# Performance work log

Measured on AMD Instinct MI355X. Metric: run time of the kernel, lower is better.

Reference implementation:

```python
import jax, jax.numpy as jnp
import numpy as np

N_NODES = 100000


def _sage_conv(x, src, dst, wn, ws, b):
    # mean-aggregate neighbor messages at destination nodes
    msgs = x[src]                                        # [E, D] gather
    agg = jax.ops.segment_sum(msgs, dst, num_segments=N_NODES)
    deg = jax.ops.segment_sum(jnp.ones((src.shape[0],), x.dtype), dst,
                              num_segments=N_NODES)
    agg = agg / jnp.maximum(deg, 1.0)[:, None]
    return agg @ wn + x @ ws + b


def setup_inputs() -> dict:
    key = jax.random.key(0)
    k = jax.random.split(key, 5)
    D = 128
    E = 1600000
    EL = 200000
    return {
        "node_features": jax.random.normal(k[0], (N_NODES, D), jnp.float32),
        "edge_index": jax.random.randint(k[1], (2, E), 0, N_NODES, jnp.int64),
        "edge_label_index": jax.random.randint(k[2], (2, EL), 0, N_NODES, jnp.int64),
        "w_neigh": jax.random.normal(k[3], (3, D, D), jnp.float32) * (1.0 / np.sqrt(D)),
        "w_self": jax.random.normal(k[4], (3, D, D), jnp.float32) * (1.0 / np.sqrt(D)),
        "bias": jnp.zeros((3, D), jnp.float32),
    }


def reference(node_features, edge_index, edge_label_index, w_neigh, w_self, bias):
    src, dst = edge_index[0], edge_index[1]
    # layer 0: conv -> relu (dropout is identity in eval mode)
    h = _sage_conv(node_features, src, dst, w_neigh[0], w_self[0], bias[0])
    h = jax.nn.relu(h)
    # middle layer: conv + residual -> relu
    h = jax.nn.relu(_sage_conv(h, src, dst, w_neigh[1], w_self[1], bias[1]) + h)
    # last layer: conv + residual (hidden_dim == output_dim, no projection)
    h = _sage_conv(h, src, dst, w_neigh[2], w_self[2], bias[2]) + h
    # dot-product link decoder
    logits = jnp.sum(h[edge_label_index[0]] * h[edge_label_index[1]], axis=-1)
    return logits
```

## Files before the change

kernel.cpp:

```cpp
#include <hip/hip_runtime.h>
#include <cstdint>
#include <cstddef>

#define D 128

typedef _Float16 half8 __attribute__((ext_vector_type(8)));
typedef float f32x4 __attribute__((ext_vector_type(4)));

static __device__ __forceinline__ unsigned short f2h_bits(float f) {
    union { _Float16 h; unsigned short u; } c;
    c.h = (_Float16)f;
    return c.u;
}

__global__ void hist_kernel(const int* __restrict__ dst, int E,
                            int* __restrict__ counts) {
    int i = blockIdx.x * blockDim.x + threadIdx.x;
    if (i < E) atomicAdd(&counts[dst[i]], 1);
}

__global__ void block_sum_kernel(const int* __restrict__ counts, int n,
                                 int* __restrict__ bsum) {
    __shared__ int sh[256];
    int t = threadIdx.x;
    int i = blockIdx.x * 256 + t;
    sh[t] = (i < n) ? counts[i] : 0;
    __syncthreads();
    for (int off = 128; off; off >>= 1) {
        if (t < off) sh[t] += sh[t + off];
        __syncthreads();
    }
    if (t == 0) bsum[blockIdx.x] = sh[0];
}

__global__ void scan_small_kernel(int* __restrict__ bsum, int nb,
                                  int* __restrict__ row_ptr, int N, int E) {
    __shared__ int sh[512];
    int t = threadIdx.x;
    int v = (t < nb) ? bsum[t] : 0;
    sh[t] = v;
    __syncthreads();
    for (int off = 1; off < 512; off <<= 1) {
        int add = (t >= off) ? sh[t - off] : 0;
        __syncthreads();
        sh[t] += add;
        __syncthreads();
    }
    if (t < nb) bsum[t] = sh[t] - v;
    if (t == 0) row_ptr[N] = E;
}

__global__ void block_scan_kernel(const int* __restrict__ counts, int n,
                                  const int* __restrict__ bsum,
                                  int* __restrict__ row_ptr) {
    __shared__ int sh[256];
    int t = threadIdx.x;
    int i = blockIdx.x * 256 + t;
    int v = (i < n) ? counts[i] : 0;
    sh[t] = v;
    __syncthreads();
    for (int off = 1; off < 256; off <<= 1) {
        int add = (t >= off) ? sh[t - off] : 0;
        __syncthreads();
        sh[t] += add;
        __syncthreads();
    }
    if (i < n) row_ptr[i] = bsum[blockIdx.x] + sh[t] - v;
}

__global__ void fill_kernel(const int* __restrict__ src,
                            const int* __restrict__ dst, int E,
                            const int* __restrict__ row_ptr,
                            int* __restrict__ cursor,
                            int* __restrict__ csr_src) {
    int i = blockIdx.x * blockDim.x + threadIdx.x;
    if (i < E) {
        int d = dst[i];
        int pos = row_ptr[d] + atomicAdd(&cursor[d], 1);
        csr_src[pos] = src[i];
    }
}

__global__ void f32_to_f16(const float* __restrict__ in,
                           unsigned short* __restrict__ out, int n8) {
    int i = blockIdx.x * 256 + threadIdx.x;
    if (i >= n8) return;
    float4 f0 = ((const float4*)in)[2 * i];
    float4 f1 = ((const float4*)in)[2 * i + 1];
    union { unsigned short u[8]; uint4 v; } o;
    o.u[0] = f2h_bits(f0.x); o.u[1] = f2h_bits(f0.y);
    o.u[2] = f2h_bits(f0.z); o.u[3] = f2h_bits(f0.w);
    o.u[4] = f2h_bits(f1.x); o.u[5] = f2h_bits(f1.y);
    o.u[6] = f2h_bits(f1.z); o.u[7] = f2h_bits(f1.w);
    ((uint4*)out)[i] = o.v;
}

__global__ __launch_bounds__(256) void gather_agg16(
    const unsigned short* __restrict__ h16, const int* __restrict__ row_ptr,
    const int* __restrict__ csr_src,
    unsigned short* __restrict__ agg16, int N) {
    int node = (int)((blockIdx.x * (size_t)blockDim.x + threadIdx.x) >> 6);
    int lane = threadIdx.x & 63;
    if (node >= N) return;
    int beg = row_ptr[node], end = row_ptr[node + 1];
    const int col = lane * 2;
    float ax[8], ay[8];
#pragma unroll
    for (int j = 0; j < 8; j++) { ax[j] = 0.f; ay[j] = 0.f; }
    int e = beg;
    for (; e + 8 <= end; e += 8) {
        int s[8];
#pragma unroll
        for (int j = 0; j < 8; j++) s[j] = csr_src[e + j];
        unsigned int v[8];
#pragma unroll
        for (int j = 0; j < 8; j++)
            v[j] = *(const unsigned int*)(h16 + (size_t)s[j] * D + col);
#pragma unroll
        for (int j = 0; j < 8; j++) {
            union { unsigned int u; _Float16 h[2]; } c; c.u = v[j];
            ax[j] += (float)c.h[0];
            ay[j] += (float)c.h[1];
        }
    }
    for (; e < end; ++e) {
        int s = csr_src[e];
        union { unsigned int u; _Float16 h[2]; } c;
        c.u = *(const unsigned int*)(h16 + (size_t)s * D + col);
        ax[0] += (float)c.h[0];
        ay[0] += (float)c.h[1];
    }
    float sx = (ax[0] + ax[1]) + (ax[2] + ax[3]) + (ax[4] + ax[5]) + (ax[6] + ax[7]);
    float sy = (ay[0] + ay[1]) + (ay[2] + ay[3]) + (ay[4] + ay[5]) + (ay[6] + ay[7]);
    float sc = 1.0f / fmaxf((float)(end - beg), 1.0f);
    union { unsigned int u; _Float16 h[2]; } o;
    o.h[0] = (_Float16)(sx * sc);
    o.h[1] = (_Float16)(sy * sc);
    *(unsigned int*)(agg16 + (size_t)node * D + col) = o.u;
}

__global__ void wprep_kernel(const float* __restrict__ wn,
                             const float* __restrict__ wsf,
                             unsigned short* __restrict__ wh,
                             unsigned short* __restrict__ wl) {
    int idx = blockIdx.x * 256 + threadIdx.x;
    int L = idx >> 15;
    int rem = idx & 32767;
    int n = rem >> 8;
    int k = rem & 255;
    float w = (k < 128) ? wn[L * 16384 + k * 128 + n]
                        : wsf[L * 16384 + (k - 128) * 128 + n];
    _Float16 hi = (_Float16)w;
    _Float16 lo = (_Float16)(w - (float)hi);
    union { _Float16 h; unsigned short u; } ch, cl;
    ch.h = hi; cl.h = lo;
    wh[idx] = ch.u;
    wl[idx] = cl.u;
}

template <bool RELU, bool RES, bool F32OUT>
__global__ __launch_bounds__(256) void gemm_mfma16(
    const unsigned short* __restrict__ agg16,
    const unsigned short* __restrict__ h16self,
    const unsigned short* __restrict__ res16,
    const unsigned short* __restrict__ wh,
    const unsigned short* __restrict__ wl,
    const float* __restrict__ bias,
    float* __restrict__ hout,
    unsigned short* __restrict__ h16out,
    int N) {
    const int t = threadIdx.x;
    const int wv = t >> 6;
    const int lane = t & 63;
    const int r = lane & 15;
    const int q = lane >> 4;
    const int m0 = blockIdx.x * 128 + (wv >> 1) * 64;
    const int n0 = (wv & 1) * 64;

    int rowA[4];
#pragma unroll
    for (int mt = 0; mt < 4; mt++) {
        int rr = m0 + mt * 16 + r;
        rowA[mt] = (rr < N) ? rr : (N - 1);
    }

    f32x4 acc[4][4];
#pragma unroll
    for (int mt = 0; mt < 4; mt++)
#pragma unroll
        for (int nt = 0; nt < 4; nt++) acc[mt][nt] = (f32x4){0.f, 0.f, 0.f, 0.f};

#pragma unroll
    for (int kb = 0; kb < 8; kb++) {
        const unsigned short* base = (kb < 4) ? agg16 : h16self;
        const int ko = (kb & 3) * 32 + q * 8;
        half8 a[4];
#pragma unroll
        for (int mt = 0; mt < 4; mt++)
            a[mt] = *(const half8*)(base + (size_t)rowA[mt] * D + ko);
        const int wko = kb * 32 + q * 8;
#pragma unroll
        for (int nt = 0; nt < 4; nt++) {
            const size_t wo = (size_t)(n0 + nt * 16 + r) * 256 + wko;
            half8 whv = *(const half8*)(wh + wo);
            half8 wlv = *(const half8*)(wl + wo);
#pragma unroll
            for (int mt = 0; mt < 4; mt++) {
                acc[mt][nt] = __builtin_amdgcn_mfma_f32_16x16x32_f16(
                    a[mt], whv, acc[mt][nt], 0, 0, 0);
                acc[mt][nt] = __builtin_amdgcn_mfma_f32_16x16x32_f16(
                    a[mt], wlv, acc[mt][nt], 0, 0, 0);
            }
        }
    }

#pragma unroll
    for (int nt = 0; nt < 4; nt++) {
        const int col = n0 + nt * 16 + r;
        const float bv = bias[col];
#pragma unroll
        for (int mt = 0; mt < 4; mt++) {
#pragma unroll
            for (int reg = 0; reg < 4; reg++) {
                int row = m0 + mt * 16 + q * 4 + reg;
                if (row >= N) continue;
                float o = acc[mt][nt][reg] + bv;
                if (RES)
                    o += (float)(*(const _Float16*)(res16 + (size_t)row * D + col));
                if (RELU) o = fmaxf(o, 0.f);
                if (F32OUT) hout[(size_t)row * D + col] = o;
                else        h16out[(size_t)row * D + col] = f2h_bits(o);
            }
        }
    }
}

__global__ void decoder_kernel(const float* __restrict__ h,
                               const int* __restrict__ eli, int EL,
                               float* __restrict__ out) {
    long long tid = (long long)blockIdx.x * blockDim.x + threadIdx.x;
    int lane = (int)(tid & 31);
    long long e = tid >> 5;
    if (e >= EL) return;
    int u = eli[e];
    int v = eli[e + EL];
    float4 a = *(const float4*)(h + (long long)u * D + lane * 4);
    float4 b = *(const float4*)(h + (long long)v * D + lane * 4);
    float p = a.x * b.x + a.y * b.y + a.z * b.z + a.w * b.w;
#pragma unroll
    for (int off = 16; off; off >>= 1) p += __shfl_xor(p, off);
    if (lane == 0) out[e] = p;
}

static inline size_t align256(size_t x) { return (x + 255) & ~(size_t)255; }

extern "C" void kernel_launch(void* const* d_in, const int* in_sizes, int n_in,
                              void* d_out, int out_size, void* d_ws,
                              size_t ws_size, hipStream_t stream) {
    const float* x    = (const float*)d_in[0];
    const int*   ei   = (const int*)d_in[1];
    const int*   eli  = (const int*)d_in[2];
    const float* wn   = (const float*)d_in[3];
    const float* wsf  = (const float*)d_in[4];
    const float* bias = (const float*)d_in[5];

    const int N  = in_sizes[0] / D;
    const int E  = in_sizes[1] / 2;
    const int EL = in_sizes[2] / 2;

    const int* src = ei;
    const int* dst = ei + E;

    char* p = (char*)d_ws;
    int*   counts  = (int*)p;   p += align256((size_t)N * sizeof(int));
    int*   row_ptr = (int*)p;   p += align256((size_t)(N + 1) * sizeof(int));
    int*   bsum    = (int*)p;   p += align256((size_t)1024 * sizeof(int));
    unsigned short* wh  = (unsigned short*)p; p += align256((size_t)3 * 32768 * 2);
    unsigned short* wl  = (unsigned short*)p; p += align256((size_t)3 * 32768 * 2);
    int*   csr_src = (int*)p;   p += align256((size_t)E * sizeof(int));
    unsigned short* x16   = (unsigned short*)p; p += align256((size_t)N * D * 2);
    unsigned short* h1    = (unsigned short*)p; p += align256((size_t)N * D * 2);
    unsigned short* h2    = (unsigned short*)p; p += align256((size_t)N * D * 2);
    unsigned short* agg16 = (unsigned short*)p; p += align256((size_t)N * D * 2);
    float* hA      = (float*)p;

    const int nb = (N + 255) / 256;
    const int eb = (E + 255) / 256;
    const int tile_blocks = (N + 127) / 128;
    const int gather_blocks = (N + 3) / 4;
    const int n8 = N * D / 8;

    wprep_kernel<<<384, 256, 0, stream>>>(wn, wsf, wh, wl);
    f32_to_f16<<<(n8 + 255) / 256, 256, 0, stream>>>(x, x16, n8);

    hipMemsetAsync(counts, 0, (size_t)N * sizeof(int), stream);
    hist_kernel<<<eb, 256, 0, stream>>>(dst, E, counts);
    block_sum_kernel<<<nb, 256, 0, stream>>>(counts, N, bsum);
    scan_small_kernel<<<1, 512, 0, stream>>>(bsum, nb, row_ptr, N, E);
    block_scan_kernel<<<nb, 256, 0, stream>>>(counts, N, bsum, row_ptr);
    hipMemsetAsync(counts, 0, (size_t)N * sizeof(int), stream);
    fill_kernel<<<eb, 256, 0, stream>>>(src, dst, E, row_ptr, counts, csr_src);

    gather_agg16<<<gather_blocks, 256, 0, stream>>>(x16, row_ptr, csr_src, agg16, N);
    gemm_mfma16<true, false, false><<<tile_blocks, 256, 0, stream>>>(
        agg16, x16, nullptr, wh + 0 * 32768, wl + 0 * 32768, bias + 0 * D,
        nullptr, h1, N);

    gather_agg16<<<gather_blocks, 256, 0, stream>>>(h1, row_ptr, csr_src, agg16, N);
    gemm_mfma16<true, true, false><<<tile_blocks, 256, 0, stream>>>(
        agg16, h1, h1, wh + 1 * 32768, wl + 1 * 32768, bias + 1 * D,
        nullptr, h2, N);

    gather_agg16<<<gather_blocks, 256, 0, stream>>>(h2, row_ptr, csr_src, agg16, N);
    gemm_mfma16<false, true, true><<<tile_blocks, 256, 0, stream>>>(
        agg16, h2, h2, wh + 2 * 32768, wl + 2 * 32768, bias + 2 * D,
        hA, nullptr, N);

    decoder_kernel<<<(int)(((long long)EL * 32 + 255) / 256), 256, 0, stream>>>(
        hA, eli, EL, (float*)d_out);
}
```

Before: 715.1 us.

## Prefetch GEMM operands one k-step ahead, pre-pack weights per lane, drop memset

The GEMM kernel now loads the next k-block's activation and weight fragments into registers while the MFMA instructions run on the current block, so load latency can overlap compute. Weights are pre-packed in MFMA lane order so each lane reads one contiguous 16-byte chunk. The fill kernel now counts down with atomicSub on the histogram counts, which removes the second memset. The cost is higher register pressure from the double-buffered fragments, which may lower occupancy.

```diff
diff --git a/kernel.cpp b/kernel.cpp
--- a/kernel.cpp
+++ b/kernel.cpp
@@ -71,12 +71,12 @@
 __global__ void fill_kernel(const int* __restrict__ src,
                             const int* __restrict__ dst, int E,
                             const int* __restrict__ row_ptr,
-                            int* __restrict__ cursor,
+                            int* __restrict__ counts,
                             int* __restrict__ csr_src) {
     int i = blockIdx.x * blockDim.x + threadIdx.x;
     if (i < E) {
         int d = dst[i];
-        int pos = row_ptr[d] + atomicAdd(&cursor[d], 1);
+        int pos = row_ptr[d] + atomicSub(&counts[d], 1) - 1;
         csr_src[pos] = src[i];
     }
 }
@@ -141,21 +141,31 @@
 
 __global__ void wprep_kernel(const float* __restrict__ wn,
                              const float* __restrict__ wsf,
-                             unsigned short* __restrict__ wh,
-                             unsigned short* __restrict__ wl) {
-    int idx = blockIdx.x * 256 + threadIdx.x;
-    int L = idx >> 15;
-    int rem = idx & 32767;
-    int n = rem >> 8;
-    int k = rem & 255;
-    float w = (k < 128) ? wn[L * 16384 + k * 128 + n]
-                        : wsf[L * 16384 + (k - 128) * 128 + n];
-    _Float16 hi = (_Float16)w;
-    _Float16 lo = (_Float16)(w - (float)hi);
-    union { _Float16 h; unsigned short u; } ch, cl;
-    ch.h = hi; cl.h = lo;
-    wh[idx] = ch.u;
-    wl[idx] = cl.u;
+                             unsigned short* __restrict__ whp,
+                             unsigned short* __restrict__ wlp) {
+    int tid = blockIdx.x * 256 + threadIdx.x;
+    if (tid >= 12288) return;
+    int lane = tid & 63;
+    int kb = (tid >> 6) & 7;
+    int nb = (tid >> 9) & 7;
+    int L  = tid >> 12;
+    int n = nb * 16 + (lane & 15);
+    int kbase = kb * 32 + (lane >> 4) * 8;
+    union { unsigned short u[8]; uint4 v; } oh, ol;
+#pragma unroll
+    for (int j = 0; j < 8; j++) {
+        int k = kbase + j;
+        float w = (k < 128) ? wn[L * 16384 + k * 128 + n]
+                            : wsf[L * 16384 + (k - 128) * 128 + n];
+        _Float16 hi = (_Float16)w;
+        _Float16 lo = (_Float16)(w - (float)hi);
+        union { _Float16 h; unsigned short u; } ch, cl;
+        ch.h = hi; cl.h = lo;
+        oh.u[j] = ch.u;
+        ol.u[j] = cl.u;
+    }
+    ((uint4*)whp)[tid] = oh.v;
+    ((uint4*)wlp)[tid] = ol.v;
 }
 
 template <bool RELU, bool RES, bool F32OUT>
@@ -163,8 +173,8 @@
     const unsigned short* __restrict__ agg16,
     const unsigned short* __restrict__ h16self,
     const unsigned short* __restrict__ res16,
-    const unsigned short* __restrict__ wh,
-    const unsigned short* __restrict__ wl,
+    const unsigned short* __restrict__ whp,
+    const unsigned short* __restrict__ wlp,
     const float* __restrict__ bias,
     float* __restrict__ hout,
     unsigned short* __restrict__ h16out,
@@ -175,7 +185,7 @@
     const int r = lane & 15;
     const int q = lane >> 4;
     const int m0 = blockIdx.x * 128 + (wv >> 1) * 64;
-    const int n0 = (wv & 1) * 64;
+    const int nhalf = wv & 1;
 
     int rowA[4];
 #pragma unroll
@@ -184,39 +194,66 @@
         rowA[mt] = (rr < N) ? rr : (N - 1);
     }
 
+    const unsigned short* whL = whp + lane * 8;
+    const unsigned short* wlL = wlp + lane * 8;
+
     f32x4 acc[4][4];
 #pragma unroll
     for (int mt = 0; mt < 4; mt++)
 #pragma unroll
         for (int nt = 0; nt < 4; nt++) acc[mt][nt] = (f32x4){0.f, 0.f, 0.f, 0.f};
 
+    half8 aC[4], aN[4], whC[4], whN[4], wlC[4], wlN[4];
+
+    {
+        const int ko = q * 8;
+#pragma unroll
+        for (int mt = 0; mt < 4; mt++)
+            aC[mt] = *(const half8*)(agg16 + (size_t)rowA[mt] * D + ko);
+#pragma unroll
+        for (int nt = 0; nt < 4; nt++) {
+            const size_t wo = (size_t)(((nhalf * 4 + nt) * 8 + 0) << 9);
+            whC[nt] = *(const half8*)(whL + wo);
+            wlC[nt] = *(const half8*)(wlL + wo);
+        }
+    }
+
 #pragma unroll
     for (int kb = 0; kb < 8; kb++) {
-        const unsigned short* base = (kb < 4) ? agg16 : h16self;
-        const int ko = (kb & 3) * 32 + q * 8;
-        half8 a[4];
-#pragma unroll
-        for (int mt = 0; mt < 4; mt++)
-            a[mt] = *(const half8*)(base + (size_t)rowA[mt] * D + ko);
-        const int wko = kb * 32 + q * 8;
+        if (kb < 7) {
+            const unsigned short* nbase = ((kb + 1) < 4) ? agg16 : h16self;
+            const int ko = ((kb + 1) & 3) * 32 + q * 8;
+#pragma unroll
+            for (int mt = 0; mt < 4; mt++)
+                aN[mt] = *(const half8*)(nbase + (size_t)rowA[mt] * D + ko);
+#pragma unroll
+            for (int nt = 0; nt < 4; nt++) {
+                const size_t wo = (size_t)(((nhalf * 4 + nt) * 8 + (kb + 1)) << 9);
+                whN[nt] = *(const half8*)(whL + wo);
+                wlN[nt] = *(const half8*)(wlL + wo);
+            }
+        }
 #pragma unroll
         for (int nt = 0; nt < 4; nt++) {
-            const size_t wo = (size_t)(n0 + nt * 16 + r) * 256 + wko;
-            half8 whv = *(const half8*)(wh + wo);
-            half8 wlv = *(const half8*)(wl + wo);
 #pragma unroll
             for (int mt = 0; mt < 4; mt++) {
                 acc[mt][nt] = __builtin_amdgcn_mfma_f32_16x16x32_f16(
-                    a[mt], whv, acc[mt][nt], 0, 0, 0);
+                    aC[mt], whC[nt], acc[mt][nt], 0, 0, 0);
                 acc[mt][nt] = __builtin_amdgcn_mfma_f32_16x16x32_f16(
-                    a[mt], wlv, acc[mt][nt], 0, 0, 0);
+                    aC[mt], wlC[nt], acc[mt][nt], 0, 0, 0);
             }
         }
+        if (kb < 7) {
+#pragma unroll
+            for (int mt = 0; mt < 4; mt++) aC[mt] = aN[mt];
+#pragma unroll
+            for (int nt = 0; nt < 4; nt++) { whC[nt] = whN[nt]; wlC[nt] = wlN[nt]; }
+        }
     }
 
 #pragma unroll
     for (int nt = 0; nt < 4; nt++) {
-        const int col = n0 + nt * 16 + r;
+        const int col = nhalf * 64 + nt * 16 + r;
         const float bv = bias[col];
 #pragma unroll
         for (int mt = 0; mt < 4; mt++) {
@@ -275,8 +312,8 @@
     int*   counts  = (int*)p;   p += align256((size_t)N * sizeof(int));
     int*   row_ptr = (int*)p;   p += align256((size_t)(N + 1) * sizeof(int));
     int*   bsum    = (int*)p;   p += align256((size_t)1024 * sizeof(int));
-    unsigned short* wh  = (unsigned short*)p; p += align256((size_t)3 * 32768 * 2);
-    unsigned short* wl  = (unsigned short*)p; p += align256((size_t)3 * 32768 * 2);
+    unsigned short* whp = (unsigned short*)p; p += align256((size_t)3 * 32768 * 2);
+    unsigned short* wlp = (unsigned short*)p; p += align256((size_t)3 * 32768 * 2);
     int*   csr_src = (int*)p;   p += align256((size_t)E * sizeof(int));
     unsigned short* x16   = (unsigned short*)p; p += align256((size_t)N * D * 2);
     unsigned short* h1    = (unsigned short*)p; p += align256((size_t)N * D * 2);
@@ -290,7 +327,7 @@
     const int gather_blocks = (N + 3) / 4;
     const int n8 = N * D / 8;
 
-    wprep_kernel<<<384, 256, 0, stream>>>(wn, wsf, wh, wl);
+    wprep_kernel<<<48, 256, 0, stream>>>(wn, wsf, whp, wlp);
     f32_to_f16<<<(n8 + 255) / 256, 256, 0, stream>>>(x, x16, n8);
 
     hipMemsetAsync(counts, 0, (size_t)N * sizeof(int), stream);
@@ -298,22 +335,21 @@
     block_sum_kernel<<<nb, 256, 0, stream>>>(counts, N, bsum);
     scan_small_kernel<<<1, 512, 0, stream>>>(bsum, nb, row_ptr, N, E);
     block_scan_kernel<<<nb, 256, 0, stream>>>(counts, N, bsum, row_ptr);
-    hipMemsetAsync(counts, 0, (size_t)N * sizeof(int), stream);
     fill_kernel<<<eb, 256, 0, stream>>>(src, dst, E, row_ptr, counts, csr_src);
 
     gather_agg16<<<gather_blocks, 256, 0, stream>>>(x16, row_ptr, csr_src, agg16, N);
     gemm_mfma16<true, false, false><<<tile_blocks, 256, 0, stream>>>(
-        agg16, x16, nullptr, wh + 0 * 32768, wl + 0 * 32768, bias + 0 * D,
+        agg16, x16, nullptr, whp + 0 * 32768, wlp + 0 * 32768, bias + 0 * D,
         nullptr, h1, N);
 
     gather_agg16<<<gather_blocks, 256, 0, stream>>>(h1, row_ptr, csr_src, agg16, N);
     gemm_mfma16<true, true, false><<<tile_blocks, 256, 0, stream>>>(
-        agg16, h1, h1, wh + 1 * 32768, wl + 1 * 32768, bias + 1 * D,
+        agg16, h1, h1, whp + 1 * 32768, wlp + 1 * 32768, bias + 1 * D,
         nullptr, h2, N);
 
     gather_agg16<<<gather_blocks, 256, 0, stream>>>(h2, row_ptr, csr_src, agg16, N);
     gemm_mfma16<false, true, true><<<tile_blocks, 256, 0, stream>>>(
-        agg16, h2, h2, wh + 2 * 32768, wl + 2 * 32768, bias + 2 * D,
+        agg16, h2, h2, whp + 2 * 32768, wlp + 2 * 32768, bias + 2 * D,
         hA, nullptr, N);
 
     decoder_kernel<<<(int)(((long long)EL * 32 + 255) / 256), 256, 0, stream>>>(
```

Measured after the change: 658.8 us. 1.09x faster.
